# Kernel optimization log

Measured on AMD Instinct MI355X. Metric: run time of the kernel, lower is better.

## Reference

```python
import jax, jax.numpy as jnp
import numpy as np
from jax import lax


def setup_inputs() -> dict:
    key = jax.random.key(0)
    k = jax.random.split(key, 5)
    B, L, ntaps, C = 128, 16384, 128, 128
    return {
        "x": jax.random.normal(k[0], (B, 1, L), dtype=jnp.float32),
        "conv_w": jax.random.normal(k[1], (C, 1, 3), dtype=jnp.float32) * 0.1,
        "conv_b": jax.random.normal(k[2], (C,), dtype=jnp.float32) * 0.1,
        "fc_w": jax.random.normal(k[3], (ntaps, C), dtype=jnp.float32) * 0.05,
        "fc_b": jax.random.normal(k[4], (ntaps,), dtype=jnp.float32) * 0.05,
        "ntaps": ntaps,
    }


def reference(x, conv_w, conv_b, fc_w, fc_b, ntaps):
    # ---- Localiser: Conv1d(1,128,3,padding=1) -> AdaptiveAvgPool1d(1) -> Linear(128, ntaps)
    h = lax.conv_general_dilated(
        x, conv_w, window_strides=(1,), padding=[(1, 1)],
        dimension_numbers=("NCH", "OIH", "NCH"))  # [B,128,L]
    h = h + conv_b[None, :, None]
    pooled = jnp.mean(h, axis=2)                  # [B,128]
    filt = pooled @ fc_w.T + fc_b                 # [B,ntaps]

    # ---- adaptive_filter: per-sample conv1d via groups=B, padding=ntaps
    B = x.shape[0]
    xr = jnp.transpose(x, (1, 0, 2))              # [1,B,L] (batch as channels)
    w = filt[:, None, :]                          # [B,1,ntaps]
    y = lax.conv_general_dilated(
        xr, w, window_strides=(1,), padding=[(ntaps, ntaps)],
        dimension_numbers=("NCH", "OIH", "NCH"),
        feature_group_count=B)                    # [1,B,L+ntaps+1]
    return jnp.transpose(y, (1, 0, 2))            # [B,1,L+ntaps+1]
```

## Files before the change

### kernel.cpp

```cpp
#include <hip/hip_runtime.h>

#define LEN   16384
#define NB    128
#define NC    128
#define NTAPS 128
#define LOUT  16513
#define NT    13
#define SPAN  (NT*256 + 144)

typedef __attribute__((ext_vector_type(8))) short bf16x8;
typedef __attribute__((ext_vector_type(4))) float f32x4;


__device__ __forceinline__ unsigned short f2bf(float f) {
    union { float f; unsigned u; } c; c.f = f;
    unsigned r = c.u + 0x7FFF + ((c.u >> 16) & 1);
    return (unsigned short)(r >> 16);
}

__global__ __launch_bounds__(256) void prep_kernel(
    const float* __restrict__ x, const float* __restrict__ conv_w,
    const float* __restrict__ conv_b, const float* __restrict__ fc_w,
    const float* __restrict__ fc_b, float* __restrict__ ws)
{
    const int blk = blockIdx.x;
    const int tid = threadIdx.x;
    if (blk < 2 * NB) {
        const float4* x4 = reinterpret_cast<const float4*>(x)
                         + (blk >> 1) * (LEN / 4) + (blk & 1) * (LEN / 8);
        float s = 0.f;
        #pragma unroll
        for (int i = 0; i < 8; ++i) {
            float4 v = x4[tid + i * 256];
            s += (v.x + v.y) + (v.z + v.w);
        }
        #pragma unroll
        for (int off = 32; off > 0; off >>= 1) s += __shfl_down(s, off, 64);
        __shared__ float part[4];
        if ((tid & 63) == 0) part[tid >> 6] = s;
        __syncthreads();
        if (tid == 0) ws[blk] = (part[0] + part[1]) + (part[2] + part[3]);
    } else {
        if (tid < NTAPS) {
            float g0 = 0.f, g1 = 0.f, g2 = 0.f, h = fc_b[tid];
            for (int c = 0; c < NC; ++c) {
                float f = fc_w[tid * NC + c];
                g0 = fmaf(f, conv_w[c * 3 + 0], g0);
                g1 = fmaf(f, conv_w[c * 3 + 1], g1);
                g2 = fmaf(f, conv_w[c * 3 + 2], g2);
                h  = fmaf(f, conv_b[c], h);
            }
            ws[256 + tid] = g0;
            ws[384 + tid] = g1;
            ws[512 + tid] = g2;
            ws[640 + tid] = h;
        }
    }
}

__global__ __launch_bounds__(256) void fir_mfma(
    const float* __restrict__ x, const float* __restrict__ ws,
    float* __restrict__ out)
{
    const int b   = blockIdx.y;
    const int tid = threadIdx.x;
    const int Tbase = blockIdx.x * NT;

    __shared__ unsigned short sxp[SPAN];
    __shared__ unsigned short fp[288];

    const float Sb = ws[2 * b] + ws[2 * b + 1];
    const float x0 = x[(size_t)b * LEN];
    const float xl = x[(size_t)b * LEN + LEN - 1];

    const int P0 = Tbase * 256;
    const float4* xr4 = reinterpret_cast<const float4*>(x) + (size_t)b * (LEN / 4);
    #pragma unroll
    for (int r = 0; r < 4; ++r) {
        int i = tid + r * 256;
        if (i < SPAN / 4) {
            int g4 = (P0 >> 2) + i - 32;
            float4 v = make_float4(0.f, 0.f, 0.f, 0.f);
            if (g4 >= 0 && g4 < LEN / 4) v = xr4[g4];
            ushort4 hv;
            hv.x = f2bf(v.x); hv.y = f2bf(v.y); hv.z = f2bf(v.z); hv.w = f2bf(v.w);
            *reinterpret_cast<ushort4*>(&sxp[4 * i]) = hv;
        }
    }

    if (tid < 128) {
        const float g0 = ws[256 + tid], g1 = ws[384 + tid];
        const float g2 = ws[512 + tid], hh = ws[640 + tid];
        const float invL = 1.0f / (float)LEN;
        float f = hh + invL * fmaf(Sb - xl, g0, fmaf(Sb, g1, (Sb - x0) * g2));
        fp[128 + tid] = f2bf(f);
    } else {
        fp[tid - 128] = 0;
        if (tid < 160) fp[tid + 128] = 0;
    }
    __syncthreads();

    const int l = tid & 63, w = tid >> 6;
    const int n = l & 15;
    const int g = l >> 4;
    bf16x8 afrag[5];
    #pragma unroll
    for (int kb = 0; kb < 5; ++kb)
        #pragma unroll
        for (int hf = 0; hf < 2; ++hf)
            #pragma unroll
            for (int j = 0; j < 4; ++j)
                afrag[kb][hf * 4 + j] =
                    (short)fp[128 + 32 * kb + 16 * hf + 4 * g + j - n];

    float* orow = out + (size_t)b * LOUT;
    #pragma unroll
    for (int it = 0; it < 4; ++it) {
        const int tau = it * 4 + w;
        if (tau >= NT) break;
        const int T = Tbase + tau;
        const unsigned short* bp = &sxp[tau * 256 + 16 * n + 4 * g];
        f32x4 acc = {0.f, 0.f, 0.f, 0.f};
        #pragma unroll
        for (int kb = 0; kb < 5; ++kb) {
            ushort4 lo = *reinterpret_cast<const ushort4*>(bp + 32 * kb);
            ushort4 hi = *reinterpret_cast<const ushort4*>(bp + 32 * kb + 16);
            bf16x8 bfrag;
            bfrag[0] = (short)lo.x; bfrag[1] = (short)lo.y;
            bfrag[2] = (short)lo.z; bfrag[3] = (short)lo.w;
            bfrag[4] = (short)hi.x; bfrag[5] = (short)hi.y;
            bfrag[6] = (short)hi.z; bfrag[7] = (short)hi.w;
            acc = __builtin_amdgcn_mfma_f32_16x16x32_bf16(afrag[kb], bfrag, acc, 0, 0, 0);
        }
        const int t0 = 256 * T + 16 * n + 4 * g;
        if (T < 64) {
            orow[t0 + 0] = acc[0];
            orow[t0 + 1] = acc[1];
            orow[t0 + 2] = acc[2];
            orow[t0 + 3] = acc[3];
        } else {
            #pragma unroll
            for (int j = 0; j < 4; ++j)
                if (t0 + j < LOUT) orow[t0 + j] = acc[j];
        }
    }
}

extern "C" void kernel_launch(void* const* d_in, const int* in_sizes, int n_in,
                              void* d_out, int out_size, void* d_ws, size_t ws_size,
                              hipStream_t stream)
{
    const float* x      = (const float*)d_in[0];
    const float* conv_w = (const float*)d_in[1];
    const float* conv_b = (const float*)d_in[2];
    const float* fc_w   = (const float*)d_in[3];
    const float* fc_b   = (const float*)d_in[4];
    float* ws  = (float*)d_ws;
    float* out = (float*)d_out;

    prep_kernel<<<dim3(2 * NB + 1), 256, 0, stream>>>(x, conv_w, conv_b, fc_w, fc_b, ws);

    dim3 grid(5, NB);
    fir_mfma<<<grid, 256, 0, stream>>>(x, ws, out);
}
```

Before: 19.66 us.

## Fuse prep and FIR kernels into one launch with per-block redundant reductions

Merges the separate mean-reduction and filter-folding prep kernel into the FIR kernel, so each block computes the full row sum and the folded fc/conv weights itself. The grid shrinks to 2 blocks of 512 threads per batch row, and each block covers 33 tiles. This removes a kernel launch and the workspace round-trip. In exchange every block reads the whole row plus fc_w redundantly, and there are far fewer blocks (256) to hide latency.

```diff
diff --git a/kernel.cpp b/kernel.cpp
--- a/kernel.cpp
+++ b/kernel.cpp
@@ -2,15 +2,13 @@
 
 #define LEN   16384
 #define NB    128
-#define NC    128
 #define NTAPS 128
 #define LOUT  16513
-#define NT    13
+#define NT    33
 #define SPAN  (NT*256 + 144)
 
 typedef __attribute__((ext_vector_type(8))) short bf16x8;
 typedef __attribute__((ext_vector_type(4))) float f32x4;
-
 
 __device__ __forceinline__ unsigned short f2bf(float f) {
     union { float f; unsigned u; } c; c.f = f;
@@ -18,86 +16,95 @@
     return (unsigned short)(r >> 16);
 }
 
-__global__ __launch_bounds__(256) void prep_kernel(
+__global__ __launch_bounds__(512) void fused_fir(
     const float* __restrict__ x, const float* __restrict__ conv_w,
     const float* __restrict__ conv_b, const float* __restrict__ fc_w,
-    const float* __restrict__ fc_b, float* __restrict__ ws)
-{
-    const int blk = blockIdx.x;
-    const int tid = threadIdx.x;
-    if (blk < 2 * NB) {
-        const float4* x4 = reinterpret_cast<const float4*>(x)
-                         + (blk >> 1) * (LEN / 4) + (blk & 1) * (LEN / 8);
-        float s = 0.f;
-        #pragma unroll
-        for (int i = 0; i < 8; ++i) {
-            float4 v = x4[tid + i * 256];
-            s += (v.x + v.y) + (v.z + v.w);
-        }
-        #pragma unroll
-        for (int off = 32; off > 0; off >>= 1) s += __shfl_down(s, off, 64);
-        __shared__ float part[4];
-        if ((tid & 63) == 0) part[tid >> 6] = s;
-        __syncthreads();
-        if (tid == 0) ws[blk] = (part[0] + part[1]) + (part[2] + part[3]);
-    } else {
-        if (tid < NTAPS) {
-            float g0 = 0.f, g1 = 0.f, g2 = 0.f, h = fc_b[tid];
-            for (int c = 0; c < NC; ++c) {
-                float f = fc_w[tid * NC + c];
-                g0 = fmaf(f, conv_w[c * 3 + 0], g0);
-                g1 = fmaf(f, conv_w[c * 3 + 1], g1);
-                g2 = fmaf(f, conv_w[c * 3 + 2], g2);
-                h  = fmaf(f, conv_b[c], h);
-            }
-            ws[256 + tid] = g0;
-            ws[384 + tid] = g1;
-            ws[512 + tid] = g2;
-            ws[640 + tid] = h;
-        }
-    }
-}
-
-__global__ __launch_bounds__(256) void fir_mfma(
-    const float* __restrict__ x, const float* __restrict__ ws,
-    float* __restrict__ out)
+    const float* __restrict__ fc_b, float* __restrict__ out)
 {
     const int b   = blockIdx.y;
+    const int h   = blockIdx.x;
     const int tid = threadIdx.x;
-    const int Tbase = blockIdx.x * NT;
 
     __shared__ unsigned short sxp[SPAN];
     __shared__ unsigned short fp[288];
+    __shared__ float scw[384];
+    __shared__ float scb[128];
+    __shared__ float sfb[128];
+    __shared__ float parts[8];
+    __shared__ float sx0, sxl;
 
-    const float Sb = ws[2 * b] + ws[2 * b + 1];
-    const float x0 = x[(size_t)b * LEN];
-    const float xl = x[(size_t)b * LEN + LEN - 1];
+    const float* xr  = x + (size_t)b * LEN;
+    const float4* xr4 = reinterpret_cast<const float4*>(xr);
 
-    const int P0 = Tbase * 256;
-    const float4* xr4 = reinterpret_cast<const float4*>(x) + (size_t)b * (LEN / 4);
+    if (tid < 384) scw[tid] = conv_w[tid];
+    else if (tid < 512) scb[tid - 384] = conv_b[tid - 384];
+    if (tid < 128) sfb[tid] = fc_b[tid];
+    if (tid == 0) { sx0 = xr[0]; sxl = xr[LEN - 1]; }
+
+    float s = 0.f;
+    const int sbase = 32 - 2112 * h;
     #pragma unroll
-    for (int r = 0; r < 4; ++r) {
-        int i = tid + r * 256;
-        if (i < SPAN / 4) {
-            int g4 = (P0 >> 2) + i - 32;
-            float4 v = make_float4(0.f, 0.f, 0.f, 0.f);
-            if (g4 >= 0 && g4 < LEN / 4) v = xr4[g4];
+    for (int p = 0; p < 8; ++p) {
+        const int g4 = tid + p * 512;
+        float4 v = xr4[g4];
+        s += (v.x + v.y) + (v.z + v.w);
+        const int s4 = g4 + sbase;
+        if (s4 >= 0 && s4 < SPAN / 4) {
             ushort4 hv;
             hv.x = f2bf(v.x); hv.y = f2bf(v.y); hv.z = f2bf(v.z); hv.w = f2bf(v.w);
-            *reinterpret_cast<ushort4*>(&sxp[4 * i]) = hv;
+            *reinterpret_cast<ushort4*>(&sxp[4 * s4]) = hv;
+        }
+    }
+    {
+        const ushort4 z = {0, 0, 0, 0};
+        if (h == 0) {
+            if (tid < 32) *reinterpret_cast<ushort4*>(&sxp[4 * tid]) = z;
+        } else {
+            if (tid < 132) *reinterpret_cast<ushort4*>(&sxp[4 * (2016 + tid)]) = z;
         }
     }
 
-    if (tid < 128) {
-        const float g0 = ws[256 + tid], g1 = ws[384 + tid];
-        const float g2 = ws[512 + tid], hh = ws[640 + tid];
+    const int t = tid >> 2, q = tid & 3;
+    const float4* fw4 = reinterpret_cast<const float4*>(fc_w);
+    float4 fw[8];
+    #pragma unroll
+    for (int m = 0; m < 8; ++m) fw[m] = fw4[8 * tid + m];
+
+    #pragma unroll
+    for (int off = 32; off > 0; off >>= 1) s += __shfl_down(s, off, 64);
+    if ((tid & 63) == 0) parts[tid >> 6] = s;
+    __syncthreads();
+    float Sb = 0.f;
+    #pragma unroll
+    for (int i = 0; i < 8; ++i) Sb += parts[i];
+
+    float g0 = 0.f, g1 = 0.f, g2 = 0.f, hh = 0.f;
+    #pragma unroll
+    for (int m = 0; m < 8; ++m) {
+        const float fv[4] = {fw[m].x, fw[m].y, fw[m].z, fw[m].w};
+        #pragma unroll
+        for (int jj = 0; jj < 4; ++jj) {
+            const int c = 32 * q + 4 * m + jj;
+            const float f = fv[jj];
+            g0 = fmaf(f, scw[3 * c + 0], g0);
+            g1 = fmaf(f, scw[3 * c + 1], g1);
+            g2 = fmaf(f, scw[3 * c + 2], g2);
+            hh = fmaf(f, scb[c], hh);
+        }
+    }
+    g0 += __shfl_xor(g0, 1); g0 += __shfl_xor(g0, 2);
+    g1 += __shfl_xor(g1, 1); g1 += __shfl_xor(g1, 2);
+    g2 += __shfl_xor(g2, 1); g2 += __shfl_xor(g2, 2);
+    hh += __shfl_xor(hh, 1); hh += __shfl_xor(hh, 2);
+
+    if (q == 0) {
         const float invL = 1.0f / (float)LEN;
-        float f = hh + invL * fmaf(Sb - xl, g0, fmaf(Sb, g1, (Sb - x0) * g2));
-        fp[128 + tid] = f2bf(f);
-    } else {
-        fp[tid - 128] = 0;
-        if (tid < 160) fp[tid + 128] = 0;
+        const float flt = sfb[t] + hh
+            + invL * fmaf(Sb - sxl, g0, fmaf(Sb, g1, (Sb - sx0) * g2));
+        fp[128 + t] = f2bf(flt);
     }
+    if (q == 1) fp[t] = 0;
+    if (q == 2 && t < 32) fp[256 + t] = 0;
     __syncthreads();
 
     const int l = tid & 63, w = tid >> 6;
@@ -115,10 +122,11 @@
 
     float* orow = out + (size_t)b * LOUT;
     #pragma unroll
-    for (int it = 0; it < 4; ++it) {
-        const int tau = it * 4 + w;
+    for (int it = 0; it < 5; ++it) {
+        const int tau = w + 8 * it;
         if (tau >= NT) break;
-        const int T = Tbase + tau;
+        const int T = h * NT + tau;
+        if (T >= 65) break;
         const unsigned short* bp = &sxp[tau * 256 + 16 * n + 4 * g];
         f32x4 acc = {0.f, 0.f, 0.f, 0.f};
         #pragma unroll
@@ -155,11 +163,8 @@
     const float* conv_b = (const float*)d_in[2];
     const float* fc_w   = (const float*)d_in[3];
     const float* fc_b   = (const float*)d_in[4];
-    float* ws  = (float*)d_ws;
     float* out = (float*)d_out;
 
-    prep_kernel<<<dim3(2 * NB + 1), 256, 0, stream>>>(x, conv_w, conv_b, fc_w, fc_b, ws);
-
-    dim3 grid(5, NB);
-    fir_mfma<<<grid, 256, 0, stream>>>(x, ws, out);
+    dim3 grid(2, NB);
+    fused_fir<<<grid, 512, 0, stream>>>(x, conv_w, conv_b, fc_w, fc_b, out);
 }
```

Measured after the change: 17.99 us (median of 2 runs). 1.09x faster.
